# Optimization experiments

Measured on AMD Instinct MI355X. Metric: run time of the kernel, lower is better.

The kernel has to match this reference:

```python
import jax, jax.numpy as jnp
import numpy as np

T, B, I, H, O = 4096, 256, 2, 32, 1


def setup_inputs() -> dict:
    key = jax.random.key(0)
    ks = jax.random.split(key, 8)
    s = 1.0 / np.sqrt(H)  # torch GRU/Linear init scale
    u = lambda k, shape: jax.random.uniform(k, shape, jnp.float32, -s, s)
    return {
        "x": jax.random.normal(ks[0], (T, B, I), jnp.float32),
        "w_ih": u(ks[1], (3 * H, I)),   # rows ordered [r, z, n] as in torch
        "w_hh": u(ks[2], (3 * H, H)),
        "b_ih": u(ks[3], (3 * H,)),
        "b_hh": u(ks[4], (3 * H,)),
        "w_fc": u(ks[5], (O, H)),
        "b_fc": u(ks[6], (O,)),
    }


def _gru_all_hidden(x, w_ih, w_hh, b_ih, b_hh):
    # Precompute input projections for all steps in one big GEMM: (T,B,3H)
    xg = jnp.einsum('tbi,gi->tbg', x, w_ih) + b_ih

    def step(h, xg_t):
        hg = h @ w_hh.T + b_hh                      # (B,3H)
        xr, xz, xn = jnp.split(xg_t, 3, axis=-1)
        hr, hz, hn = jnp.split(hg, 3, axis=-1)
        r = jax.nn.sigmoid(xr + hr)
        z = jax.nn.sigmoid(xz + hz)
        n = jnp.tanh(xn + r * hn)
        h_new = (1.0 - z) * n + z * h
        return h_new, h_new

    h0 = jnp.zeros((x.shape[1], w_hh.shape[1]), x.dtype)
    _, hs = jax.lax.scan(step, h0, xg)
    return hs                                       # (T,B,H)


def reference(x, w_ih, w_hh, b_ih, b_hh, w_fc, b_fc):
    hs = _gru_all_hidden(x, w_ih, w_hh, b_ih, b_hh)  # (T,B,H)
    # Faithful to the source: output[:, -1, :] with batch_first=False picks
    # the last batch element's hidden state at every timestep -> (T,H)
    out = hs[:, -1, :]
    return out @ w_fc.T + b_fc                       # (T,O)
```

## Files before the change

kernel.cpp:

```cpp
#include <hip/hip_runtime.h>


#define TT 4096

typedef float v2f __attribute__((ext_vector_type(2)));

__device__ __forceinline__ v2f fma2(v2f a, v2f b, v2f c) {
    return __builtin_elementwise_fma(a, b, c);
}
__device__ __forceinline__ float rl(float v, int l) {
    return __int_as_float(__builtin_amdgcn_readlane(__float_as_int(v), l));
}
__device__ __forceinline__ float fexp2(float x) { return __builtin_amdgcn_exp2f(x); }
__device__ __forceinline__ float frcp(float x)  { return __builtin_amdgcn_rcpf(x); }

#define NLOG2E  (-1.44269504088896340736f)
#define TLOG2E  ( 2.88539008177792681472f)

__global__ __launch_bounds__(64, 1)
__attribute__((amdgpu_waves_per_eu(1, 1)))
void gru_seq(
    const float* __restrict__ x,
    const float* __restrict__ w_ih,
    const float* __restrict__ w_hh,
    const float* __restrict__ b_ih,
    const float* __restrict__ b_hh,
    float* __restrict__ hbuf)
{
    __shared__ float hsm[64];

    const int lane = threadIdx.x;
    const int low  = lane & 31;
    const int row0 = lane;
    const int row1 = 64 + low;
    const bool lo_half = lane < 32;

    const v2f* w_hh2 = (const v2f*)w_hh;
    v2f w0[16], w1[16];
#pragma unroll
    for (int k = 0; k < 16; ++k) w0[k] = w_hh2[row0 * 16 + k] * NLOG2E;
#pragma unroll
    for (int k = 0; k < 16; ++k) w1[k] = w_hh2[row1 * 16 + k] * TLOG2E;

    const float wi00 = w_ih[row0 * 2 + 0] * NLOG2E;
    const float wi01 = w_ih[row0 * 2 + 1] * NLOG2E;
    const float wi10 = w_ih[row1 * 2 + 0] * TLOG2E;
    const float wi11 = w_ih[row1 * 2 + 1] * TLOG2E;
    const float bias0 = (b_ih[row0] + b_hh[row0]) * NLOG2E;
    const float bi1   = b_ih[row1] * TLOG2E;
    const float bh1   = b_hh[row1] * TLOG2E;

    hsm[lane] = 0.0f;
    float h_el = 0.0f;
    float hacc[4];

    const float2* xp = (const float2*)x;
    float2 xv = xp[(size_t)lane * 256 + 255];

    const float4* h4 = (const float4*)hsm;

    for (int tb = 0; tb < 64; ++tb) {
        float2 xv_next = xv;
        if (tb < 63) xv_next = xp[((size_t)(tb + 1) * 64 + lane) * 256 + 255];
        float4* hout = (float4*)(hbuf + (size_t)low * TT + tb * 64);

#pragma unroll 4
        for (int i = 0; i < 64; ++i) {
            const float x0 = rl(xv.x, i);
            const float x1 = rl(xv.y, i);
            const float base0 = fmaf(x1, wi01, fmaf(x0, wi00, bias0));
            const float xn    = fmaf(x1, wi11, fmaf(x0, wi10, bi1));

            float4 hq[8];
#pragma unroll
            for (int k = 0; k < 8; ++k) hq[k] = h4[k];

            v2f arz0 = {base0, 0.0f}, arz1 = {0.0f, 0.0f};
            v2f an0  = {bh1,   0.0f}, an1  = {0.0f, 0.0f};
#pragma unroll
            for (int k = 0; k < 8; ++k) {
                v2f hl = {hq[k].x, hq[k].y};
                v2f hh = {hq[k].z, hq[k].w};
                arz0 = fma2(hl, w0[2 * k],     arz0);
                arz1 = fma2(hh, w0[2 * k + 1], arz1);
                an0  = fma2(hl, w1[2 * k],     an0);
                an1  = fma2(hh, w1[2 * k + 1], an1);
            }
            v2f srz = arz0 + arz1;
            v2f sn  = an0 + an1;
            const float pre_s = srz.x + srz.y;
            const float hn_s  = sn.x + sn.y;

            const float sg    = frcp(1.0f + fexp2(pre_s));
            const float other = __shfl_xor(sg, 32);
            const float rr = lo_half ? sg : other;
            const float zz = lo_half ? other : sg;

            const float nv = fmaf(-2.0f, frcp(1.0f + fexp2(fmaf(rr, hn_s, xn))), 1.0f);
            h_el = fmaf(zz, h_el - nv, nv);

            hsm[lane] = h_el;
            hacc[i & 3] = h_el;
            if ((i & 3) == 3) hout[i >> 2] = *(const float4*)hacc;
        }
        xv = xv_next;
    }
}

__global__ void fc_out(const float* __restrict__ hbuf,
                       const float* __restrict__ w_fc,
                       const float* __restrict__ b_fc,
                       float* __restrict__ out)
{
    const int t = blockIdx.x * blockDim.x + threadIdx.x;
    if (t >= TT) return;
    float acc = 0.f;
#pragma unroll
    for (int j = 0; j < 32; ++j) acc = fmaf(hbuf[j * TT + t], w_fc[j], acc);
    out[t] = acc + b_fc[0];
}

extern "C" void kernel_launch(void* const* d_in, const int* in_sizes, int n_in,
                              void* d_out, int out_size, void* d_ws, size_t ws_size,
                              hipStream_t stream) {
    const float* x    = (const float*)d_in[0];
    const float* w_ih = (const float*)d_in[1];
    const float* w_hh = (const float*)d_in[2];
    const float* b_ih = (const float*)d_in[3];
    const float* b_hh = (const float*)d_in[4];
    const float* w_fc = (const float*)d_in[5];
    const float* b_fc = (const float*)d_in[6];
    float* out  = (float*)d_out;
    float* hbuf = (float*)d_ws;

    gru_seq<<<1, 64, 0, stream>>>(x, w_ih, w_hh, b_ih, b_hh, hbuf);
    fc_out<<<TT / 256, 256, 0, stream>>>(hbuf, w_fc, b_fc, out);
}
```

Before: 771.8 us.

## Replace LDS hidden-state broadcast with DPP butterfly exchange and per-lane gates

Each lane now computes all three gates (r, z, n) for one hidden unit, so the cross-half shuffle between gate results is no longer needed. The hidden state is exchanged through a tree of DPP lane permutations instead of an LDS store and vector reload, with the weight columns permuted to match the butterfly order. The upper 16 elements are rebuilt from the swizzled z and n values of the previous step, so that half of the exchange can overlap with the first half of the matvec. This aims to take LDS latency and the barrier-like dependency off the serial recurrence, at the cost of more DPP moves and a third of the FMAs done redundantly across the two half-waves.

Result: slower. 983.4 us (+27.4%).

```diff
diff --git a/kernel.cpp b/kernel.cpp
--- a/kernel.cpp
+++ b/kernel.cpp
@@ -13,6 +13,17 @@
 }
 __device__ __forceinline__ float fexp2(float x) { return __builtin_amdgcn_exp2f(x); }
 __device__ __forceinline__ float frcp(float x)  { return __builtin_amdgcn_rcpf(x); }
+__device__ __forceinline__ float keep(float x)  { asm("" : "+v"(x)); return x; }
+
+#define DPP_X1  0xB1
+#define DPP_X2  0x4E
+#define DPP_X7  0x141
+#define DPP_X15 0x140
+
+template<int CTRL>
+__device__ __forceinline__ float dppf(float x) {
+    return __int_as_float(__builtin_amdgcn_mov_dpp(__float_as_int(x), CTRL, 0xF, 0xF, false));
+}
 
 #define NLOG2E  (-1.44269504088896340736f)
 #define TLOG2E  ( 2.88539008177792681472f)
@@ -27,37 +38,55 @@
     const float* __restrict__ b_hh,
     float* __restrict__ hbuf)
 {
-    __shared__ float hsm[64];
-
     const int lane = threadIdx.x;
     const int low  = lane & 31;
-    const int row0 = lane;
-    const int row1 = 64 + low;
-    const bool lo_half = lane < 32;
-
-    const v2f* w_hh2 = (const v2f*)w_hh;
-    v2f w0[16], w1[16];
-#pragma unroll
-    for (int k = 0; k < 16; ++k) w0[k] = w_hh2[row0 * 16 + k] * NLOG2E;
-#pragma unroll
-    for (int k = 0; k < 16; ++k) w1[k] = w_hh2[row1 * 16 + k] * TLOG2E;
-
-    const float wi00 = w_ih[row0 * 2 + 0] * NLOG2E;
-    const float wi01 = w_ih[row0 * 2 + 1] * NLOG2E;
-    const float wi10 = w_ih[row1 * 2 + 0] * TLOG2E;
-    const float wi11 = w_ih[row1 * 2 + 1] * TLOG2E;
-    const float bias0 = (b_ih[row0] + b_hh[row0]) * NLOG2E;
-    const float bi1   = b_ih[row1] * TLOG2E;
-    const float bh1   = b_hh[row1] * TLOG2E;
-
-    hsm[lane] = 0.0f;
-    float h_el = 0.0f;
+    const int rrow = low;
+    const int zrow = 32 + low;
+    const int nrow = 64 + low;
+
+    int sig[32];
+#pragma unroll
+    for (int i2 = 0; i2 < 32; ++i2) {
+        int b = i2 & 15;
+        int s = (i2 & 16) ? 16 : 0;
+        if (b & 1) s ^= 15;
+        if (b & 2) s ^= 7;
+        if (b & 4) s ^= 2;
+        if (b & 8) s ^= 1;
+        sig[i2] = s;
+    }
+
+    v2f wr[16], wz[16], wn[16];
+#pragma unroll
+    for (int p = 0; p < 16; ++p) {
+        const int c0 = low ^ sig[2 * p], c1 = low ^ sig[2 * p + 1];
+        v2f a = { w_hh[rrow * 32 + c0], w_hh[rrow * 32 + c1] };
+        v2f b = { w_hh[zrow * 32 + c0], w_hh[zrow * 32 + c1] };
+        v2f c = { w_hh[nrow * 32 + c0], w_hh[nrow * 32 + c1] };
+        a *= NLOG2E;  b *= NLOG2E;  c *= TLOG2E;
+        wr[p].x = keep(a.x); wr[p].y = keep(a.y);
+        wz[p].x = keep(b.x); wz[p].y = keep(b.y);
+        wn[p].x = keep(c.x); wn[p].y = keep(c.y);
+    }
+    const float wir0 = keep(w_ih[rrow * 2 + 0] * NLOG2E);
+    const float wir1 = keep(w_ih[rrow * 2 + 1] * NLOG2E);
+    const float wiz0 = keep(w_ih[zrow * 2 + 0] * NLOG2E);
+    const float wiz1 = keep(w_ih[zrow * 2 + 1] * NLOG2E);
+    const float win0 = keep(w_ih[nrow * 2 + 0] * TLOG2E);
+    const float win1 = keep(w_ih[nrow * 2 + 1] * TLOG2E);
+    const float bsr  = keep((b_ih[rrow] + b_hh[rrow]) * NLOG2E);
+    const float bsz  = keep((b_ih[zrow] + b_hh[zrow]) * NLOG2E);
+    const float bin_ = keep(b_ih[nrow] * TLOG2E);
+    const float bhn  = keep(b_hh[nrow] * TLOG2E);
+
+    float h_el   = 0.0f;
+    float g1prev = 0.0f;
+    float zz16   = 0.0f;
+    float nv16   = 0.0f;
     float hacc[4];
 
     const float2* xp = (const float2*)x;
     float2 xv = xp[(size_t)lane * 256 + 255];
-
-    const float4* h4 = (const float4*)hsm;
 
     for (int tb = 0; tb < 64; ++tb) {
         float2 xv_next = xv;
@@ -66,40 +95,75 @@
 
 #pragma unroll 4
         for (int i = 0; i < 64; ++i) {
+            float t0[16];
+            t0[0] = h_el;
+            t0[1] = dppf<DPP_X15>(t0[0]);
+            t0[2] = dppf<DPP_X7>(t0[0]);  t0[3] = dppf<DPP_X7>(t0[1]);
+#pragma unroll
+            for (int b = 0; b < 4; ++b) t0[4 + b] = dppf<DPP_X2>(t0[b]);
+#pragma unroll
+            for (int b = 0; b < 8; ++b) t0[8 + b] = dppf<DPP_X1>(t0[b]);
+
             const float x0 = rl(xv.x, i);
             const float x1 = rl(xv.y, i);
-            const float base0 = fmaf(x1, wi01, fmaf(x0, wi00, bias0));
-            const float xn    = fmaf(x1, wi11, fmaf(x0, wi10, bi1));
-
-            float4 hq[8];
-#pragma unroll
-            for (int k = 0; k < 8; ++k) hq[k] = h4[k];
-
-            v2f arz0 = {base0, 0.0f}, arz1 = {0.0f, 0.0f};
-            v2f an0  = {bh1,   0.0f}, an1  = {0.0f, 0.0f};
-#pragma unroll
-            for (int k = 0; k < 8; ++k) {
-                v2f hl = {hq[k].x, hq[k].y};
-                v2f hh = {hq[k].z, hq[k].w};
-                arz0 = fma2(hl, w0[2 * k],     arz0);
-                arz1 = fma2(hh, w0[2 * k + 1], arz1);
-                an0  = fma2(hl, w1[2 * k],     an0);
-                an1  = fma2(hh, w1[2 * k + 1], an1);
+            const float br = fmaf(x1, wir1, fmaf(x0, wir0, bsr));
+            const float bz = fmaf(x1, wiz1, fmaf(x0, wiz0, bsz));
+            const float xn = fmaf(x1, win1, fmaf(x0, win0, bin_));
+
+            v2f ar0 = {br,  0.0f}, ar1 = {0.0f, 0.0f};
+            v2f az0 = {bz,  0.0f}, az1 = {0.0f, 0.0f};
+            v2f an0 = {bhn, 0.0f}, an1 = {0.0f, 0.0f};
+#pragma unroll
+            for (int p = 0; p < 8; p += 2) {
+                v2f ha = {t0[2 * p],     t0[2 * p + 1]};
+                v2f hb = {t0[2 * p + 2], t0[2 * p + 3]};
+                ar0 = fma2(ha, wr[p],     ar0);
+                ar1 = fma2(hb, wr[p + 1], ar1);
+                az0 = fma2(ha, wz[p],     az0);
+                az1 = fma2(hb, wz[p + 1], az1);
+                an0 = fma2(ha, wn[p],     an0);
+                an1 = fma2(hb, wn[p + 1], an1);
             }
-            v2f srz = arz0 + arz1;
-            v2f sn  = an0 + an1;
-            const float pre_s = srz.x + srz.y;
-            const float hn_s  = sn.x + sn.y;
-
-            const float sg    = frcp(1.0f + fexp2(pre_s));
-            const float other = __shfl_xor(sg, 32);
-            const float rr = lo_half ? sg : other;
-            const float zz = lo_half ? other : sg;
+
+            const float g1 = fmaf(zz16, g1prev - nv16, nv16);
+            g1prev = g1;
+            float t1[16];
+            t1[0] = g1;
+            t1[1] = dppf<DPP_X15>(t1[0]);
+            t1[2] = dppf<DPP_X7>(t1[0]);  t1[3] = dppf<DPP_X7>(t1[1]);
+#pragma unroll
+            for (int b = 0; b < 4; ++b) t1[4 + b] = dppf<DPP_X2>(t1[b]);
+#pragma unroll
+            for (int b = 0; b < 8; ++b) t1[8 + b] = dppf<DPP_X1>(t1[b]);
+
+#pragma unroll
+            for (int p = 0; p < 8; p += 2) {
+                v2f ha = {t1[2 * p],     t1[2 * p + 1]};
+                v2f hb = {t1[2 * p + 2], t1[2 * p + 3]};
+                ar0 = fma2(ha, wr[8 + p],     ar0);
+                ar1 = fma2(hb, wr[8 + p + 1], ar1);
+                az0 = fma2(ha, wz[8 + p],     az0);
+                az1 = fma2(hb, wz[8 + p + 1], az1);
+                an0 = fma2(ha, wn[8 + p],     an0);
+                an1 = fma2(hb, wn[8 + p + 1], an1);
+            }
+
+            v2f sr = ar0 + ar1;
+            v2f sz = az0 + az1;
+            v2f sn = an0 + an1;
+            const float pr   = sr.x + sr.y;
+            const float pz   = sz.x + sz.y;
+            const float hn_s = sn.x + sn.y;
+
+            const float rr = frcp(1.0f + fexp2(pr));
+            const float zz = frcp(1.0f + fexp2(pz));
+            zz16 = __int_as_float(__builtin_amdgcn_ds_swizzle(__float_as_int(zz), 0x401F));
 
             const float nv = fmaf(-2.0f, frcp(1.0f + fexp2(fmaf(rr, hn_s, xn))), 1.0f);
+            nv16 = __int_as_float(__builtin_amdgcn_ds_swizzle(__float_as_int(nv), 0x401F));
+
             h_el = fmaf(zz, h_el - nv, nv);
 
-            hsm[lane] = h_el;
             hacc[i & 3] = h_el;
             if ((i & 3) == 3) hout[i >> 2] = *(const float4*)hacc;
         }
```

## Compute r, z, n gates per lane to drop cross-half shuffle

Applied to the files above, without the earlier changes.

Each lane now holds all three gate weight rows for its hidden unit and computes r, z and n itself, replacing the split where the low and high halves computed r and z separately and exchanged them through a cross-lane shuffle. This removes the shuffle latency from the serial recurrence critical path. In exchange each lane does half again as many FMAs per step (three 32-wide dot products instead of two) and keeps more weight registers, pinned with empty asm to stop rematerialisation. Both wave halves now compute redundantly.

Result: slower. 865.0 us (+12.1%).

```diff
diff --git a/kernel.cpp b/kernel.cpp
--- a/kernel.cpp
+++ b/kernel.cpp
@@ -13,12 +13,13 @@
 }
 __device__ __forceinline__ float fexp2(float x) { return __builtin_amdgcn_exp2f(x); }
 __device__ __forceinline__ float frcp(float x)  { return __builtin_amdgcn_rcpf(x); }
+__device__ __forceinline__ float pin(float x)   { asm volatile("" : "+v"(x)); return x; }
 
 #define NLOG2E  (-1.44269504088896340736f)
 #define TLOG2E  ( 2.88539008177792681472f)
 
-__global__ __launch_bounds__(64, 1)
-__attribute__((amdgpu_waves_per_eu(1, 1)))
+__global__
+__attribute__((amdgpu_flat_work_group_size(64, 64), amdgpu_waves_per_eu(1, 1)))
 void gru_seq(
     const float* __restrict__ x,
     const float* __restrict__ w_ih,
@@ -31,24 +32,31 @@
 
     const int lane = threadIdx.x;
     const int low  = lane & 31;
-    const int row0 = lane;
-    const int row1 = 64 + low;
-    const bool lo_half = lane < 32;
+    const int rrow = low;
+    const int zrow = 32 + low;
+    const int nrow = 64 + low;
 
     const v2f* w_hh2 = (const v2f*)w_hh;
-    v2f w0[16], w1[16];
+    v2f wr[16], wz[16], wn[16];
 #pragma unroll
-    for (int k = 0; k < 16; ++k) w0[k] = w_hh2[row0 * 16 + k] * NLOG2E;
-#pragma unroll
-    for (int k = 0; k < 16; ++k) w1[k] = w_hh2[row1 * 16 + k] * TLOG2E;
-
-    const float wi00 = w_ih[row0 * 2 + 0] * NLOG2E;
-    const float wi01 = w_ih[row0 * 2 + 1] * NLOG2E;
-    const float wi10 = w_ih[row1 * 2 + 0] * TLOG2E;
-    const float wi11 = w_ih[row1 * 2 + 1] * TLOG2E;
-    const float bias0 = (b_ih[row0] + b_hh[row0]) * NLOG2E;
-    const float bi1   = b_ih[row1] * TLOG2E;
-    const float bh1   = b_hh[row1] * TLOG2E;
+    for (int k = 0; k < 16; ++k) {
+        v2f a = w_hh2[rrow * 16 + k] * NLOG2E;
+        v2f b = w_hh2[zrow * 16 + k] * NLOG2E;
+        v2f c = w_hh2[nrow * 16 + k] * TLOG2E;
+        wr[k].x = pin(a.x); wr[k].y = pin(a.y);
+        wz[k].x = pin(b.x); wz[k].y = pin(b.y);
+        wn[k].x = pin(c.x); wn[k].y = pin(c.y);
+    }
+    const float wir0 = pin(w_ih[rrow * 2 + 0] * NLOG2E);
+    const float wir1 = pin(w_ih[rrow * 2 + 1] * NLOG2E);
+    const float wiz0 = pin(w_ih[zrow * 2 + 0] * NLOG2E);
+    const float wiz1 = pin(w_ih[zrow * 2 + 1] * NLOG2E);
+    const float win0 = pin(w_ih[nrow * 2 + 0] * TLOG2E);
+    const float win1 = pin(w_ih[nrow * 2 + 1] * TLOG2E);
+    const float bsr  = pin((b_ih[rrow] + b_hh[rrow]) * NLOG2E);
+    const float bsz  = pin((b_ih[zrow] + b_hh[zrow]) * NLOG2E);
+    const float bin_ = pin(b_ih[nrow] * TLOG2E);
+    const float bhn  = pin(b_hh[nrow] * TLOG2E);
 
     hsm[lane] = 0.0f;
     float h_el = 0.0f;
@@ -66,35 +74,50 @@
 
 #pragma unroll 4
         for (int i = 0; i < 64; ++i) {
-            const float x0 = rl(xv.x, i);
-            const float x1 = rl(xv.y, i);
-            const float base0 = fmaf(x1, wi01, fmaf(x0, wi00, bias0));
-            const float xn    = fmaf(x1, wi11, fmaf(x0, wi10, bi1));
-
             float4 hq[8];
 #pragma unroll
             for (int k = 0; k < 8; ++k) hq[k] = h4[k];
 
-            v2f arz0 = {base0, 0.0f}, arz1 = {0.0f, 0.0f};
-            v2f an0  = {bh1,   0.0f}, an1  = {0.0f, 0.0f};
+            const float x0 = rl(xv.x, i);
+            const float x1 = rl(xv.y, i);
+            const float br = fmaf(x1, wir1, fmaf(x0, wir0, bsr));
+            const float bz = fmaf(x1, wiz1, fmaf(x0, wiz0, bsz));
+            const float xn = fmaf(x1, win1, fmaf(x0, win0, bin_));
+
+            v2f ar0 = {br, 0.0f}, ar1 = {0.0f, 0.0f};
 #pragma unroll
             for (int k = 0; k < 8; ++k) {
                 v2f hl = {hq[k].x, hq[k].y};
                 v2f hh = {hq[k].z, hq[k].w};
-                arz0 = fma2(hl, w0[2 * k],     arz0);
-                arz1 = fma2(hh, w0[2 * k + 1], arz1);
-                an0  = fma2(hl, w1[2 * k],     an0);
-                an1  = fma2(hh, w1[2 * k + 1], an1);
+                ar0 = fma2(hl, wr[2 * k],     ar0);
+                ar1 = fma2(hh, wr[2 * k + 1], ar1);
             }
-            v2f srz = arz0 + arz1;
-            v2f sn  = an0 + an1;
-            const float pre_s = srz.x + srz.y;
-            const float hn_s  = sn.x + sn.y;
+            v2f az0 = {bz, 0.0f}, az1 = {0.0f, 0.0f};
+#pragma unroll
+            for (int k = 0; k < 8; ++k) {
+                v2f hl = {hq[k].x, hq[k].y};
+                v2f hh = {hq[k].z, hq[k].w};
+                az0 = fma2(hl, wz[2 * k],     az0);
+                az1 = fma2(hh, wz[2 * k + 1], az1);
+            }
+            v2f an0 = {bhn, 0.0f}, an1 = {0.0f, 0.0f};
+#pragma unroll
+            for (int k = 0; k < 8; ++k) {
+                v2f hl = {hq[k].x, hq[k].y};
+                v2f hh = {hq[k].z, hq[k].w};
+                an0 = fma2(hl, wn[2 * k],     an0);
+                an1 = fma2(hh, wn[2 * k + 1], an1);
+            }
 
-            const float sg    = frcp(1.0f + fexp2(pre_s));
-            const float other = __shfl_xor(sg, 32);
-            const float rr = lo_half ? sg : other;
-            const float zz = lo_half ? other : sg;
+            v2f sr = ar0 + ar1;
+            v2f sz = az0 + az1;
+            v2f sn = an0 + an1;
+            const float pr   = sr.x + sr.y;
+            const float pz   = sz.x + sz.y;
+            const float hn_s = sn.x + sn.y;
+
+            const float rr = frcp(1.0f + fexp2(pr));
+            const float zz = frcp(1.0f + fexp2(pz));
 
             const float nv = fmaf(-2.0f, frcp(1.0f + fexp2(fmaf(rr, hn_s, xn))), 1.0f);
             h_el = fmaf(zz, h_el - nv, nv);
```

## Fuse FC output into GRU loop and replicate hidden-state update per lane

Applied to the files above, without the earlier changes.

Removes the separate fc_out kernel and the hbuf workspace by computing the output dot product inside the recurrent loop, writing the previous step's output from lane 0. Each lane now keeps the full 32-element hidden state in registers and recomputes it from the z and n values that lanes publish to shared memory, which replaces the cross-half shuffle and the per-lane h update. This aims to shorten the serial dependency chain per step and to drop a kernel launch, at the cost of more per-lane redundant ALU work and register pressure. Weights are pinned in registers with empty asm, and the unroll factor drops from 4 to 2.

After: 1.262 ms. +63.5%, slower.

```diff
diff --git a/kernel.cpp b/kernel.cpp
--- a/kernel.cpp
+++ b/kernel.cpp
@@ -13,46 +13,64 @@
 }
 __device__ __forceinline__ float fexp2(float x) { return __builtin_amdgcn_exp2f(x); }
 __device__ __forceinline__ float frcp(float x)  { return __builtin_amdgcn_rcpf(x); }
+__device__ __forceinline__ float pin(float x)   { asm volatile("" : "+v"(x)); return x; }
 
 #define NLOG2E  (-1.44269504088896340736f)
 #define TLOG2E  ( 2.88539008177792681472f)
 
-__global__ __launch_bounds__(64, 1)
-__attribute__((amdgpu_waves_per_eu(1, 1)))
-void gru_seq(
+__global__
+__attribute__((amdgpu_flat_work_group_size(64, 64), amdgpu_waves_per_eu(1, 1)))
+void gru_fused(
     const float* __restrict__ x,
     const float* __restrict__ w_ih,
     const float* __restrict__ w_hh,
     const float* __restrict__ b_ih,
     const float* __restrict__ b_hh,
-    float* __restrict__ hbuf)
+    const float* __restrict__ w_fc,
+    const float* __restrict__ b_fc,
+    float* __restrict__ out)
 {
     __shared__ float hsm[64];
 
     const int lane = threadIdx.x;
     const int low  = lane & 31;
+    const bool lo_half = lane < 32;
     const int row0 = lane;
     const int row1 = 64 + low;
-    const bool lo_half = lane < 32;
 
     const v2f* w_hh2 = (const v2f*)w_hh;
-    v2f w0[16], w1[16];
+    v2f wrz[16], wn[16];
 #pragma unroll
-    for (int k = 0; k < 16; ++k) w0[k] = w_hh2[row0 * 16 + k] * NLOG2E;
+    for (int k = 0; k < 16; ++k) {
+        v2f a = w_hh2[row0 * 16 + k] * NLOG2E;
+        v2f b = w_hh2[row1 * 16 + k] * TLOG2E;
+        wrz[k].x = pin(a.x); wrz[k].y = pin(a.y);
+        wn[k].x  = pin(b.x); wn[k].y  = pin(b.y);
+    }
+    const float wi00  = pin(w_ih[row0 * 2 + 0] * NLOG2E);
+    const float wi01  = pin(w_ih[row0 * 2 + 1] * NLOG2E);
+    const float wi10  = pin(w_ih[row1 * 2 + 0] * TLOG2E);
+    const float wi11  = pin(w_ih[row1 * 2 + 1] * TLOG2E);
+    const float bias0 = pin((b_ih[row0] + b_hh[row0]) * NLOG2E);
+    const float bi1   = pin(b_ih[row1] * TLOG2E);
+    const float bh1   = pin(b_hh[row1] * TLOG2E);
+
+    const v2f* wfc2 = (const v2f*)w_fc;
+    v2f wfc[16];
 #pragma unroll
-    for (int k = 0; k < 16; ++k) w1[k] = w_hh2[row1 * 16 + k] * TLOG2E;
+    for (int k = 0; k < 16; ++k) {
+        v2f c = wfc2[k];
+        wfc[k].x = pin(c.x); wfc[k].y = pin(c.y);
+    }
+    const float bfc = pin(b_fc[0]);
 
-    const float wi00 = w_ih[row0 * 2 + 0] * NLOG2E;
-    const float wi01 = w_ih[row0 * 2 + 1] * NLOG2E;
-    const float wi10 = w_ih[row1 * 2 + 0] * TLOG2E;
-    const float wi11 = w_ih[row1 * 2 + 1] * TLOG2E;
-    const float bias0 = (b_ih[row0] + b_hh[row0]) * NLOG2E;
-    const float bi1   = b_ih[row1] * TLOG2E;
-    const float bh1   = b_hh[row1] * TLOG2E;
+    v2f hp[16];
+#pragma unroll
+    for (int k = 0; k < 16; ++k) hp[k] = (v2f){0.0f, 0.0f};
 
     hsm[lane] = 0.0f;
-    float h_el = 0.0f;
-    float hacc[4];
+
+    const int paddr = lane ^ 32;
 
     const float2* xp = (const float2*)x;
     float2 xv = xp[(size_t)lane * 256 + 255];
@@ -62,62 +80,85 @@
     for (int tb = 0; tb < 64; ++tb) {
         float2 xv_next = xv;
         if (tb < 63) xv_next = xp[((size_t)(tb + 1) * 64 + lane) * 256 + 255];
-        float4* hout = (float4*)(hbuf + (size_t)low * TT + tb * 64);
 
-#pragma unroll 4
+#pragma unroll 2
         for (int i = 0; i < 64; ++i) {
+            const int t = tb * 64 + i;
+
+            float4 zq[8], nq[8];
+#pragma unroll
+            for (int k = 0; k < 8; ++k) zq[k] = h4[k];
+#pragma unroll
+            for (int k = 0; k < 8; ++k) nq[k] = h4[8 + k];
+
+#pragma unroll
+            for (int k = 0; k < 8; ++k) {
+                v2f zl = {zq[k].x, zq[k].y}, zh = {zq[k].z, zq[k].w};
+                v2f nl = {nq[k].x, nq[k].y}, nh = {nq[k].z, nq[k].w};
+                hp[2 * k]     = fma2(zl, hp[2 * k]     - nl, nl);
+                hp[2 * k + 1] = fma2(zh, hp[2 * k + 1] - nh, nh);
+            }
+
+            v2f f0 = {0.f, 0.f}, f1 = {0.f, 0.f};
+#pragma unroll
+            for (int k = 0; k < 8; ++k) {
+                f0 = fma2(hp[2 * k],     wfc[2 * k],     f0);
+                f1 = fma2(hp[2 * k + 1], wfc[2 * k + 1], f1);
+            }
+            v2f fs = f0 + f1;
+            const float ov = fs.x + fs.y + bfc;
+            if (lane == 0) out[(t + TT - 1) & (TT - 1)] = ov;
+
             const float x0 = rl(xv.x, i);
             const float x1 = rl(xv.y, i);
             const float base0 = fmaf(x1, wi01, fmaf(x0, wi00, bias0));
             const float xn    = fmaf(x1, wi11, fmaf(x0, wi10, bi1));
 
-            float4 hq[8];
-#pragma unroll
-            for (int k = 0; k < 8; ++k) hq[k] = h4[k];
-
             v2f arz0 = {base0, 0.0f}, arz1 = {0.0f, 0.0f};
             v2f an0  = {bh1,   0.0f}, an1  = {0.0f, 0.0f};
 #pragma unroll
             for (int k = 0; k < 8; ++k) {
-                v2f hl = {hq[k].x, hq[k].y};
-                v2f hh = {hq[k].z, hq[k].w};
-                arz0 = fma2(hl, w0[2 * k],     arz0);
-                arz1 = fma2(hh, w0[2 * k + 1], arz1);
-                an0  = fma2(hl, w1[2 * k],     an0);
-                an1  = fma2(hh, w1[2 * k + 1], an1);
+                arz0 = fma2(hp[2 * k],     wrz[2 * k],     arz0);
+                arz1 = fma2(hp[2 * k + 1], wrz[2 * k + 1], arz1);
+                an0  = fma2(hp[2 * k],     wn[2 * k],      an0);
+                an1  = fma2(hp[2 * k + 1], wn[2 * k + 1],  an1);
             }
             v2f srz = arz0 + arz1;
             v2f sn  = an0 + an1;
             const float pre_s = srz.x + srz.y;
             const float hn_s  = sn.x + sn.y;
 
-            const float sg    = frcp(1.0f + fexp2(pre_s));
-            const float other = __shfl_xor(sg, 32);
-            const float rr = lo_half ? sg : other;
-            const float zz = lo_half ? other : sg;
+            const float sg = frcp(1.0f + fexp2(pre_s));
+            const float nv = fmaf(-2.0f, frcp(1.0f + fexp2(fmaf(sg, hn_s, xn))), 1.0f);
 
-            const float nv = fmaf(-2.0f, frcp(1.0f + fexp2(fmaf(rr, hn_s, xn))), 1.0f);
-            h_el = fmaf(zz, h_el - nv, nv);
-
-            hsm[lane] = h_el;
-            hacc[i & 3] = h_el;
-            if ((i & 3) == 3) hout[i >> 2] = *(const float4*)hacc;
+            hsm[paddr] = lo_half ? nv : sg;
         }
         xv = xv_next;
     }
-}
 
-__global__ void fc_out(const float* __restrict__ hbuf,
-                       const float* __restrict__ w_fc,
-                       const float* __restrict__ b_fc,
-                       float* __restrict__ out)
-{
-    const int t = blockIdx.x * blockDim.x + threadIdx.x;
-    if (t >= TT) return;
-    float acc = 0.f;
+    {
+        float4 zq[8], nq[8];
 #pragma unroll
-    for (int j = 0; j < 32; ++j) acc = fmaf(hbuf[j * TT + t], w_fc[j], acc);
-    out[t] = acc + b_fc[0];
+        for (int k = 0; k < 8; ++k) zq[k] = h4[k];
+#pragma unroll
+        for (int k = 0; k < 8; ++k) nq[k] = h4[8 + k];
+#pragma unroll
+        for (int k = 0; k < 8; ++k) {
+            v2f zl = {zq[k].x, zq[k].y}, zh = {zq[k].z, zq[k].w};
+            v2f nl = {nq[k].x, nq[k].y}, nh = {nq[k].z, nq[k].w};
+            hp[2 * k]     = fma2(zl, hp[2 * k]     - nl, nl);
+            hp[2 * k + 1] = fma2(zh, hp[2 * k + 1] - nh, nh);
+        }
+        v2f f0 = {0.f, 0.f}, f1 = {0.f, 0.f};
+#pragma unroll
+        for (int k = 0; k < 8; ++k) {
+            f0 = fma2(hp[2 * k],     wfc[2 * k],     f0);
+            f1 = fma2(hp[2 * k + 1], wfc[2 * k + 1], f1);
+        }
+        v2f fs = f0 + f1;
+        const float ov = fs.x + fs.y + bfc;
+        if (lane == 0) out[TT - 1] = ov;
+    }
 }
 
 extern "C" void kernel_launch(void* const* d_in, const int* in_sizes, int n_in,
@@ -130,9 +171,7 @@
     const float* b_hh = (const float*)d_in[4];
     const float* w_fc = (const float*)d_in[5];
     const float* b_fc = (const float*)d_in[6];
-    float* out  = (float*)d_out;
-    float* hbuf = (float*)d_ws;
+    float* out = (float*)d_out;
 
-    gru_seq<<<1, 64, 0, stream>>>(x, w_ih, w_hh, b_ih, b_hh, hbuf);
-    fc_out<<<TT / 256, 256, 0, stream>>>(hbuf, w_fc, b_fc, out);
+    gru_fused<<<1, 64, 0, stream>>>(x, w_ih, w_hh, b_ih, b_hh, w_fc, b_fc, out);
 }
```
